# Performance work log

Measured on AMD Instinct MI355X. Metric: run time of the kernel, lower is better.

Reference implementation:

```python
import jax, jax.numpy as jnp
import numpy as np

N_HEAD = 12
M_HIST = 5      # Anderson history window (AndersonAcceleration.m)
BETA = 1.0      # Anderson mixing (AndersonAcceleration.beta)
LN_EPS = 1e-5


def _layer_norm(x, w, b):
    mu = x.mean(-1, keepdims=True)
    xc = x - mu
    var = (xc * xc).mean(-1, keepdims=True)
    return xc * jax.lax.rsqrt(var + LN_EPS) * w + b


def _mha(x, wqkv, bqkv, wo, bo):
    # torch nn.MultiheadAttention, batch_first, self-attention, no mask, dropout=0
    B, T, C = x.shape
    dh = C // N_HEAD
    qkv = x @ wqkv.T + bqkv                       # [B,T,3C]
    q, k, v = jnp.split(qkv, 3, axis=-1)
    def heads(t):
        return t.reshape(B, T, N_HEAD, dh).transpose(0, 2, 1, 3)  # [B,H,T,dh]
    q, k, v = heads(q), heads(k), heads(v)
    scores = jnp.einsum('bhqd,bhkd->bhqk', q, k) / jnp.sqrt(jnp.asarray(dh, x.dtype))
    att = jax.nn.softmax(scores, axis=-1)
    out = jnp.einsum('bhqk,bhkd->bhqd', att, v).transpose(0, 2, 1, 3).reshape(B, T, C)
    return out @ wo.T + bo


def _deq_delta(z, u, emb_row, ln1_w, ln1_b, in_proj_w, in_proj_b, out_proj_w,
               out_proj_b, ln2_w, ln2_b, mlp_w1, mlp_b1, mlp_w2, mlp_b2):
    # DEQOperator.forward -> delta_z
    z_temporal = z + 0.1 * emb_row                 # broadcast [C] over [B,T,C]
    z_ctx = z_temporal + u
    x = _layer_norm(z_ctx, ln1_w, ln1_b)
    attn_out = _mha(x, in_proj_w, in_proj_b, out_proj_w, out_proj_b)
    z_attn = z + attn_out
    h = _layer_norm(z_attn, ln2_w, ln2_b)
    h = jax.nn.gelu(h @ mlp_w1.T + mlp_b1, approximate=False) @ mlp_w2.T + mlp_b2
    z_mlp = z_attn + h
    return z_mlp - z


def _deq_solve(u, iter_emb, ln1_w, ln1_b, in_proj_w, in_proj_b, out_proj_w,
               out_proj_b, ln2_w, ln2_b, mlp_w1, mlp_b1, mlp_w2, mlp_b2, num_iters):
    B, T, C = u.shape
    z = jnp.zeros_like(u)
    Xs, Fs = [], []   # Anderson history of states / residuals
    max_row = iter_emb.shape[0] - 1
    for it in range(num_iters):
        emb_row = iter_emb[min(it, max_row)]
        delta = _deq_delta(z, u, emb_row, ln1_w, ln1_b, in_proj_w, in_proj_b,
                           out_proj_w, out_proj_b, ln2_w, ln2_b,
                           mlp_w1, mlp_b1, mlp_w2, mlp_b2)
        res = delta  # residual of f(z) = z + delta_z w.r.t. z
        Xs.append(z); Fs.append(res)
        if len(Xs) > M_HIST:
            Xs.pop(0); Fs.pop(0)
        if len(Xs) == 1:
            z = z + BETA * res
        else:
            K = len(Xs) - 1
            dF = jnp.stack(Fs[:-1], 0) - res[None]               # [K,B,T,C]
            dF_f = dF.transpose(1, 2, 0, 3).reshape(B * T, K, C)  # per-token LS
            r_f = res.reshape(B * T, C)
            G = jnp.einsum('nkc,nlc->nkl', dF_f, dF_f)            # [BT,K,K]
            G = G + 1e-6 * jnp.eye(K, dtype=u.dtype)
            bvec = jnp.einsum('nkc,nc->nk', dF_f, r_f)            # [BT,K]
            alpha = jnp.linalg.solve(G, bvec[..., None])[..., 0]
            d = r_f - jnp.einsum('nkc,nk->nc', dF_f, alpha)
            z = (z.reshape(B * T, C) + BETA * d).reshape(B, T, C)
    return z


def setup_inputs() -> dict:
    key = jax.random.key(0)
    ks = jax.random.split(key, 6)
    B, T, C = 4, 1024, 768
    std = 0.02
    return {
        'u': jax.random.normal(ks[0], (B, T, C), jnp.float32),
        'iter_emb': std * jax.random.normal(ks[1], (31, C), jnp.float32),
        'ln1_w': jnp.ones((C,), jnp.float32),
        'ln1_b': jnp.zeros((C,), jnp.float32),
        'in_proj_w': std * jax.random.normal(ks[2], (3 * C, C), jnp.float32),
        'in_proj_b': jnp.zeros((3 * C,), jnp.float32),
        'out_proj_w': std * jax.random.normal(ks[3], (C, C), jnp.float32),
        'out_proj_b': jnp.zeros((C,), jnp.float32),
        'ln2_w': jnp.ones((C,), jnp.float32),
        'ln2_b': jnp.zeros((C,), jnp.float32),
        'mlp_w1': std * jax.random.normal(ks[4], (4 * C, C), jnp.float32),
        'mlp_b1': jnp.zeros((4 * C,), jnp.float32),
        'mlp_w2': std * jax.random.normal(ks[5], (C, 4 * C), jnp.float32),
        'mlp_b2': jnp.zeros((C,), jnp.float32),
        'num_iters': 6,
    }


def reference(u, iter_emb, ln1_w, ln1_b, in_proj_w, in_proj_b, out_proj_w,
              out_proj_b, ln2_w, ln2_b, mlp_w1, mlp_b1, mlp_w2, mlp_b2, num_iters):
    return _deq_solve(u, iter_emb, ln1_w, ln1_b, in_proj_w, in_proj_b,
                      out_proj_w, out_proj_b, ln2_w, ln2_b,
                      mlp_w1, mlp_b1, mlp_w2, mlp_b2, int(num_iters))
```

## Files before the change

kernel.cpp:

```cpp
#include <hip/hip_runtime.h>
#include <math.h>

#define BT 4096
#define CDIM 768
#define NHEAD 12
#define DH 64
#define TSEQ 1024
#define BBATCH 4

typedef _Float16 f16;
typedef __attribute__((ext_vector_type(4))) _Float16 f16x4;
typedef __attribute__((ext_vector_type(8))) _Float16 f16x8;
typedef __attribute__((ext_vector_type(4))) float f32x4;

__device__ __forceinline__ void gload_lds16(const f16* g, f16* l) {
  __builtin_amdgcn_global_load_lds(
      (const __attribute__((address_space(1))) unsigned*)(const void*)g,
      (__attribute__((address_space(3))) unsigned*)(void*)l, 16, 0, 0);
}

__device__ __forceinline__ float block_reduce_sum(float v, float* sbuf) {
#pragma unroll
  for (int o = 32; o > 0; o >>= 1) v += __shfl_down(v, o, 64);
  int lane = threadIdx.x & 63;
  int w = threadIdx.x >> 6;
  if (lane == 0) sbuf[w] = v;
  __syncthreads();
  float r = sbuf[0] + sbuf[1] + sbuf[2] + sbuf[3];
  __syncthreads();
  return r;
}

__global__ __launch_bounds__(256) void zero_kernel(float4* __restrict__ p) {
  p[(size_t)blockIdx.x * 256 + threadIdx.x] = make_float4(0.f, 0.f, 0.f, 0.f);
}

__global__ __launch_bounds__(256) void cvt_f16_kernel(
    const float* __restrict__ in, f16* __restrict__ out) {
  size_t i = ((size_t)blockIdx.x * 256 + threadIdx.x) * 4;
  float4 v = *(const float4*)(in + i);
  f16x4 o = {(f16)v.x, (f16)v.y, (f16)v.z, (f16)v.w};
  *(f16x4*)(out + i) = o;
}

__global__ __launch_bounds__(256) void ln1_kernel(
    const float* __restrict__ z, const float* __restrict__ u,
    const float* __restrict__ emb, const float* __restrict__ w,
    const float* __restrict__ b, f16* __restrict__ x) {
  __shared__ float sbuf[4];
  int row = blockIdx.x;
  int tid = threadIdx.x;
  const float* zr = z + (size_t)row * CDIM;
  const float* ur = u + (size_t)row * CDIM;
  float v[3];
  float s = 0.f;
#pragma unroll
  for (int i = 0; i < 3; i++) {
    int c = tid + i * 256;
    v[i] = zr[c] + 0.1f * emb[c] + ur[c];
    s += v[i];
  }
  s = block_reduce_sum(s, sbuf);
  float mu = s * (1.f / CDIM);
  float sq = 0.f;
#pragma unroll
  for (int i = 0; i < 3; i++) { v[i] -= mu; sq += v[i] * v[i]; }
  sq = block_reduce_sum(sq, sbuf);
  float rstd = rsqrtf(sq * (1.f / CDIM) + 1e-5f);
  f16* xr = x + (size_t)row * CDIM;
#pragma unroll
  for (int i = 0; i < 3; i++) {
    int c = tid + i * 256;
    xr[c] = (f16)(v[i] * rstd * w[c] + b[c]);
  }
}

__global__ __launch_bounds__(256) void ln2_kernel(
    const float* __restrict__ in, const float* __restrict__ w,
    const float* __restrict__ b, f16* __restrict__ x) {
  __shared__ float sbuf[4];
  int row = blockIdx.x;
  int tid = threadIdx.x;
  const float* ir = in + (size_t)row * CDIM;
  float v[3];
  float s = 0.f;
#pragma unroll
  for (int i = 0; i < 3; i++) {
    int c = tid + i * 256;
    v[i] = ir[c];
    s += v[i];
  }
  s = block_reduce_sum(s, sbuf);
  float mu = s * (1.f / CDIM);
  float sq = 0.f;
#pragma unroll
  for (int i = 0; i < 3; i++) { v[i] -= mu; sq += v[i] * v[i]; }
  sq = block_reduce_sum(sq, sbuf);
  float rstd = rsqrtf(sq * (1.f / CDIM) + 1e-5f);
  f16* xr = x + (size_t)row * CDIM;
#pragma unroll
  for (int i = 0; i < 3; i++) {
    int c = tid + i * 256;
    xr[c] = (f16)(v[i] * rstd * w[c] + b[c]);
  }
}

__device__ __forceinline__ float gelu_exact(float t) {
  return 0.5f * t * (1.f + erff(t * 0.70710678118654752f));
}

template <int MODE>
__global__ __launch_bounds__(256, 3) void gemm_mfma(
    const f16* __restrict__ A, const f16* __restrict__ W,
    const float* __restrict__ bias, f16* __restrict__ hq,
    f16* __restrict__ hk, f16* __restrict__ hvt, f16* __restrict__ hout,
    int M, int N, int K) {
  __shared__ __align__(16) f16 As[128 * 32];
  __shared__ __align__(16) f16 Bs[128 * 32];
  int tid = threadIdx.x;
  int wv = tid >> 6, lane = tid & 63;
  int bm = blockIdx.y, bn = blockIdx.x;
  int wm = (wv >> 1) * 64, wn = (wv & 1) * 64;

  int srow = wv * 16 + (lane >> 2);
  int scol = (lane & 3) * 8;
  const f16* gA = A + (size_t)(bm * 128 + srow) * K + scol;
  const f16* gB = W + (size_t)(bn * 128 + srow) * K + scol;
  f16* lA = As + wv * 16 * 32;
  f16* lB = Bs + wv * 16 * 32;

  f32x4 acc[4][4];
#pragma unroll
  for (int i = 0; i < 4; i++)
#pragma unroll
    for (int j = 0; j < 4; j++) acc[i][j] = (f32x4){0.f, 0.f, 0.f, 0.f};

  int arow = lane & 15;
  int koff = (lane >> 4) * 8;

  for (int k0 = 0; k0 < K; k0 += 32) {
    __syncthreads();
    gload_lds16(gA + k0, lA);
    gload_lds16(gA + (size_t)64 * K + k0, lA + 64 * 32);
    gload_lds16(gB + k0, lB);
    gload_lds16(gB + (size_t)64 * K + k0, lB + 64 * 32);
    __syncthreads();
    f16x8 af[4], bfr[4];
#pragma unroll
    for (int mi = 0; mi < 4; mi++)
      af[mi] = *(const f16x8*)&As[(wm + mi * 16 + arow) * 32 + koff];
#pragma unroll
    for (int nj = 0; nj < 4; nj++)
      bfr[nj] = *(const f16x8*)&Bs[(wn + nj * 16 + arow) * 32 + koff];
#pragma unroll
    for (int mi = 0; mi < 4; mi++)
#pragma unroll
      for (int nj = 0; nj < 4; nj++)
        acc[mi][nj] = __builtin_amdgcn_mfma_f32_16x16x32_f16(
            af[mi], bfr[nj], acc[mi][nj], 0, 0, 0);
  }

  int crow0 = bm * 128 + wm + (lane >> 4) * 4;
  int ccol0 = bn * 128 + wn + (lane & 15);
#pragma unroll
  for (int nj = 0; nj < 4; nj++) {
    int col = ccol0 + nj * 16;
    float bcol = bias[col];
    if constexpr (MODE == 3) {
      int which = col / CDIM;
      int rem = col - which * CDIM;
      int h = rem >> 6;
      int d = rem & 63;
#pragma unroll
      for (int mi = 0; mi < 4; mi++) {
#pragma unroll
        for (int r = 0; r < 4; r++) {
          int m = crow0 + mi * 16 + r;
          int bb = m >> 10, t = m & 1023;
          f16 val = (f16)(acc[mi][nj][r] + bcol);
          if (which == 0)
            hq[(((size_t)(bb * NHEAD + h) * TSEQ + t) << 6) + d] = val;
          else if (which == 1)
            hk[(((size_t)(bb * NHEAD + h) * TSEQ + t) << 6) + d] = val;
          else
            hvt[(((size_t)(bb * NHEAD + h) * DH + d) << 10) + t] = val;
        }
      }
    } else {
#pragma unroll
      for (int mi = 0; mi < 4; mi++) {
#pragma unroll
        for (int r = 0; r < 4; r++) {
          int m = crow0 + mi * 16 + r;
          size_t idx = (size_t)m * N + col;
          hout[idx] = (f16)gelu_exact(acc[mi][nj][r] + bcol);
        }
      }
    }
  }
}

#define GS 72
template <int MODE>
__global__ __launch_bounds__(256, 4) void gemm_mfma64(
    const f16* __restrict__ A, const f16* __restrict__ W,
    const float* __restrict__ bias, const float* __restrict__ aux1,
    const float* __restrict__ aux2, float* __restrict__ fout0,
    int M, int N, int K) {
  __shared__ __align__(16) f16 As[64 * GS];
  __shared__ __align__(16) f16 Bs[64 * GS];
  int tid = threadIdx.x;
  int wv = tid >> 6, lane = tid & 63;
  int bm = blockIdx.x, bn = blockIdx.y;
  int wm = (wv >> 1) * 32, wn = (wv & 1) * 32;

  int srow = tid >> 2;
  int scol = (tid & 3) * 16;
  const f16* gA = A + (size_t)(bm * 64 + srow) * K + scol;
  const f16* gB = W + (size_t)(bn * 64 + srow) * K + scol;

  f32x4 acc[2][2];
#pragma unroll
  for (int i = 0; i < 2; i++)
#pragma unroll
    for (int j = 0; j < 2; j++) acc[i][j] = (f32x4){0.f, 0.f, 0.f, 0.f};

  int am = lane & 15;
  int ak = (lane >> 4) * 8;

  f16x8 a0 = *(const f16x8*)(gA);
  f16x8 a1 = *(const f16x8*)(gA + 8);
  f16x8 b0 = *(const f16x8*)(gB);
  f16x8 b1 = *(const f16x8*)(gB + 8);

  for (int k0 = 0; k0 < K; k0 += 64) {
    __syncthreads();
    *(f16x8*)&As[srow * GS + scol] = a0;
    *(f16x8*)&As[srow * GS + scol + 8] = a1;
    *(f16x8*)&Bs[srow * GS + scol] = b0;
    *(f16x8*)&Bs[srow * GS + scol + 8] = b1;
    __syncthreads();
    int kn = k0 + 64;
    if (kn < K) {
      a0 = *(const f16x8*)(gA + kn);
      a1 = *(const f16x8*)(gA + kn + 8);
      b0 = *(const f16x8*)(gB + kn);
      b1 = *(const f16x8*)(gB + kn + 8);
    }
#pragma unroll
    for (int kk = 0; kk < 2; kk++) {
      f16x8 af[2], bfr[2];
#pragma unroll
      for (int mi = 0; mi < 2; mi++)
        af[mi] = *(const f16x8*)&As[(wm + mi * 16 + am) * GS + kk * 32 + ak];
#pragma unroll
      for (int nj = 0; nj < 2; nj++)
        bfr[nj] = *(const f16x8*)&Bs[(wn + nj * 16 + am) * GS + kk * 32 + ak];
#pragma unroll
      for (int mi = 0; mi < 2; mi++)
#pragma unroll
        for (int nj = 0; nj < 2; nj++)
          acc[mi][nj] = __builtin_amdgcn_mfma_f32_16x16x32_f16(
              af[mi], bfr[nj], acc[mi][nj], 0, 0, 0);
    }
  }

  int crow0 = bm * 64 + wm + (lane >> 4) * 4;
  int ccol0 = bn * 64 + wn + (lane & 15);
#pragma unroll
  for (int nj = 0; nj < 2; nj++) {
    int col = ccol0 + nj * 16;
    float bcol = bias[col];
#pragma unroll
    for (int mi = 0; mi < 2; mi++) {
#pragma unroll
      for (int r = 0; r < 4; r++) {
        int m = crow0 + mi * 16 + r;
        size_t idx = (size_t)m * N + col;
        float val = acc[mi][nj][r] + bcol;
        if constexpr (MODE == 0) {
          fout0[idx] = val + aux1[idx];
        } else {
          fout0[idx] = val + aux1[idx] - aux2[idx];
        }
      }
    }
  }
}

#define PSTRIDE 72
#define KVS 72
__global__ __launch_bounds__(256, 3) void flash_attn8(
    const f16* __restrict__ Qg, const f16* __restrict__ Kg,
    const f16* __restrict__ Vt, f16* __restrict__ attn) {
  __shared__ __align__(16) f16 Ks[64 * KVS];
  __shared__ __align__(16) f16 Vs[64 * KVS];
  __shared__ __align__(16) f16 Plds[4][16 * PSTRIDE];
  int tid = threadIdx.x;
  int wv = tid >> 6, lane = tid & 63;
  int bh = blockIdx.x;
  int bb = bh / NHEAD, h = bh % NHEAD;
  int m0 = (blockIdx.y * 4 + wv) * 16;
  int am = lane & 15;
  int quad = lane >> 4;
  int ak = quad * 8;

  int srow = tid >> 3;
  int scol = (tid & 7) * 8;

  const f16* kb = Kg + (((size_t)bh * TSEQ) << 6);
  const f16* vb = Vt + (((size_t)bh * DH) << 10);

  const f16* qbase = Qg + (((size_t)bh * TSEQ + m0) << 6);
  f16x8 qf0 = *(const f16x8*)(qbase + am * 64 + ak);
  f16x8 qf1 = *(const f16x8*)(qbase + am * 64 + 32 + ak);
#pragma unroll
  for (int i = 0; i < 8; i++) { qf0[i] *= (f16)0.125f; qf1[i] *= (f16)0.125f; }

  f16* Pw = Plds[wv];
  f32x4 Oa[4];
#pragma unroll
  for (int i = 0; i < 4; i++) Oa[i] = (f32x4){0.f, 0.f, 0.f, 0.f};
  float lpart[4] = {0.f, 0.f, 0.f, 0.f};

  f16x8 kr0 = *(const f16x8*)(kb + (size_t)srow * 64 + scol);
  f16x8 kr1 = *(const f16x8*)(kb + (size_t)(32 + srow) * 64 + scol);
  f16x8 vr0 = *(const f16x8*)(vb + (size_t)srow * TSEQ + scol);
  f16x8 vr1 = *(const f16x8*)(vb + (size_t)(32 + srow) * TSEQ + scol);

  for (int n0 = 0; n0 < TSEQ; n0 += 64) {
    __syncthreads();
    *(f16x8*)&Ks[srow * KVS + scol] = kr0;
    *(f16x8*)&Ks[(32 + srow) * KVS + scol] = kr1;
    *(f16x8*)&Vs[srow * KVS + scol] = vr0;
    *(f16x8*)&Vs[(32 + srow) * KVS + scol] = vr1;
    __syncthreads();
    int nn = n0 + 64;
    if (nn < TSEQ) {
      kr0 = *(const f16x8*)(kb + (size_t)(nn + srow) * 64 + scol);
      kr1 = *(const f16x8*)(kb + (size_t)(nn + 32 + srow) * 64 + scol);
      vr0 = *(const f16x8*)(vb + (size_t)srow * TSEQ + nn + scol);
      vr1 = *(const f16x8*)(vb + (size_t)(32 + srow) * TSEQ + nn + scol);
    }
    f32x4 S[4];
#pragma unroll
    for (int t = 0; t < 4; t++) {
      f16x8 kf0 = *(const f16x8*)&Ks[(16 * t + am) * KVS + ak];
      f16x8 kf1 = *(const f16x8*)&Ks[(16 * t + am) * KVS + 32 + ak];
      S[t] = __builtin_amdgcn_mfma_f32_16x16x32_f16(
          qf0, kf0, (f32x4){0.f, 0.f, 0.f, 0.f}, 0, 0, 0);
      S[t] = __builtin_amdgcn_mfma_f32_16x16x32_f16(qf1, kf1, S[t], 0, 0, 0);
    }
#pragma unroll
    for (int t = 0; t < 4; t++) {
#pragma unroll
      for (int r = 0; r < 4; r++) {
        float p = __expf(S[t][r]);
        lpart[r] += p;
        Pw[(quad * 4 + r) * PSTRIDE + 16 * t + am] = (f16)p;
      }
    }
    f16x8 pa0 = *(const f16x8*)&Pw[am * PSTRIDE + ak];
    f16x8 pa1 = *(const f16x8*)&Pw[am * PSTRIDE + 32 + ak];
#pragma unroll
    for (int dt = 0; dt < 4; dt++) {
      f16x8 vf0 = *(const f16x8*)&Vs[(16 * dt + am) * KVS + ak];
      f16x8 vf1 = *(const f16x8*)&Vs[(16 * dt + am) * KVS + 32 + ak];
      Oa[dt] = __builtin_amdgcn_mfma_f32_16x16x32_f16(pa0, vf0, Oa[dt], 0, 0, 0);
      Oa[dt] = __builtin_amdgcn_mfma_f32_16x16x32_f16(pa1, vf1, Oa[dt], 0, 0, 0);
    }
  }

#pragma unroll
  for (int o = 1; o < 16; o <<= 1)
#pragma unroll
    for (int r = 0; r < 4; r++) lpart[r] += __shfl_xor(lpart[r], o, 64);

#pragma unroll
  for (int r = 0; r < 4; r++) {
    int m = m0 + quad * 4 + r;
    float inv = 1.f / lpart[r];
    f16* orow = attn + ((size_t)(bb * TSEQ + m)) * CDIM + h * DH;
#pragma unroll
    for (int dt = 0; dt < 4; dt++)
      orow[dt * 16 + am] = (f16)(Oa[dt][r] * inv);
  }
}

__global__ __launch_bounds__(256) void add_res_kernel(
    float* __restrict__ z, const float* __restrict__ r) {
  size_t i = (size_t)blockIdx.x * 256 + threadIdx.x;
  z[i] += r[i];
}

template <int KA>
__global__ __launch_bounds__(256) void anderson_kernel(
    float* __restrict__ z, const float* __restrict__ rescur,
    const float* __restrict__ p0, const float* __restrict__ p1,
    const float* __restrict__ p2, const float* __restrict__ p3) {
  __shared__ float sbuf[4];
  int row = blockIdx.x, tid = threadIdx.x;
  size_t base = (size_t)row * CDIM + tid;
  float r[3];
#pragma unroll
  for (int i = 0; i < 3; i++) r[i] = rescur[base + i * 256];
  const float* ps[4] = {p0, p1, p2, p3};
  float dF[KA][3];
#pragma unroll
  for (int k = 0; k < KA; k++)
#pragma unroll
    for (int i = 0; i < 3; i++) dF[k][i] = ps[k][base + i * 256] - r[i];

  float Gm[KA][KA], bv[KA];
#pragma unroll
  for (int k = 0; k < KA; k++) {
#pragma unroll
    for (int ll = k; ll < KA; ll++) {
      float p = 0.f;
#pragma unroll
      for (int i = 0; i < 3; i++) p += dF[k][i] * dF[ll][i];
      float t = block_reduce_sum(p, sbuf);
      Gm[k][ll] = t;
      Gm[ll][k] = t;
    }
  }
#pragma unroll
  for (int k = 0; k < KA; k++) Gm[k][k] += 1e-6f;
#pragma unroll
  for (int k = 0; k < KA; k++) {
    float p = 0.f;
#pragma unroll
    for (int i = 0; i < 3; i++) p += dF[k][i] * r[i];
    bv[k] = block_reduce_sum(p, sbuf);
  }
  float alpha[KA];
#pragma unroll
  for (int p = 0; p < KA; p++) {
    float inv = 1.f / Gm[p][p];
#pragma unroll
    for (int rr = p + 1; rr < KA; rr++) {
      float f = Gm[rr][p] * inv;
#pragma unroll
      for (int c = p; c < KA; c++) Gm[rr][c] -= f * Gm[p][c];
      bv[rr] -= f * bv[p];
    }
  }
#pragma unroll
  for (int p = KA - 1; p >= 0; p--) {
    float s2 = bv[p];
#pragma unroll
    for (int c = p + 1; c < KA; c++) s2 -= Gm[p][c] * alpha[c];
    alpha[p] = s2 / Gm[p][p];
  }
#pragma unroll
  for (int i = 0; i < 3; i++) {
    float d = r[i];
#pragma unroll
    for (int k = 0; k < KA; k++) d = fmaf(-dF[k][i], alpha[k], d);
    z[base + i * 256] += d;
  }
}

extern "C" void kernel_launch(void* const* d_in, const int* in_sizes, int n_in,
                              void* d_out, int out_size, void* d_ws,
                              size_t ws_size, hipStream_t stream) {
  (void)in_sizes; (void)n_in; (void)out_size; (void)ws_size;
  const float* u = (const float*)d_in[0];
  const float* iter_emb = (const float*)d_in[1];
  const float* ln1w = (const float*)d_in[2];
  const float* ln1b = (const float*)d_in[3];
  const float* wqkv = (const float*)d_in[4];
  const float* bqkv = (const float*)d_in[5];
  const float* wo = (const float*)d_in[6];
  const float* bo = (const float*)d_in[7];
  const float* ln2w = (const float*)d_in[8];
  const float* ln2b = (const float*)d_in[9];
  const float* w1 = (const float*)d_in[10];
  const float* b1 = (const float*)d_in[11];
  const float* w2 = (const float*)d_in[12];
  const float* b2 = (const float*)d_in[13];

  const size_t S = (size_t)BT * CDIM;
  float* ws = (float*)d_ws;
  float* z = ws + 0 * S;
  float* zattn = ws + 1 * S;
  float* res[5] = {ws + 2 * S, ws + 3 * S, ws + 4 * S, ws + 5 * S, ws + 6 * S};
  f16* q_h = (f16*)(ws + 7 * S);
  f16* k_h = q_h + S;
  f16* vt_h = q_h + 2 * S;
  f16* h_h = (f16*)(ws + 7 * S);
  f16* x_h = (f16*)(ws + 9 * S);
  f16* wqkv_h = x_h + S;
  f16* wo_h = wqkv_h + (size_t)3 * CDIM * CDIM;
  f16* w1_h = wo_h + (size_t)CDIM * CDIM;
  f16* w2_h = w1_h + (size_t)4 * CDIM * CDIM;

  cvt_f16_kernel<<<1728, 256, 0, stream>>>(wqkv, wqkv_h);
  cvt_f16_kernel<<<576, 256, 0, stream>>>(wo, wo_h);
  cvt_f16_kernel<<<2304, 256, 0, stream>>>(w1, w1_h);
  cvt_f16_kernel<<<2304, 256, 0, stream>>>(w2, w2_h);
  zero_kernel<<<S / 1024, 256, 0, stream>>>((float4*)z);

  for (int it = 0; it < 6; it++) {
    ln1_kernel<<<BT, 256, 0, stream>>>(z, u, iter_emb + it * CDIM, ln1w, ln1b,
                                       x_h);
    gemm_mfma<3><<<dim3(18, 32), 256, 0, stream>>>(
        x_h, wqkv_h, bqkv, q_h, k_h, vt_h, nullptr, BT, 3 * CDIM, CDIM);
    flash_attn8<<<dim3(BBATCH * NHEAD, TSEQ / 64), 256, 0, stream>>>(
        q_h, k_h, vt_h, x_h);
    gemm_mfma64<0><<<dim3(64, 12), 256, 0, stream>>>(
        x_h, wo_h, bo, z, nullptr, zattn, BT, CDIM, CDIM);
    ln2_kernel<<<BT, 256, 0, stream>>>(zattn, ln2w, ln2b, x_h);
    gemm_mfma<1><<<dim3(24, 32), 256, 0, stream>>>(
        x_h, w1_h, b1, nullptr, nullptr, nullptr, h_h, BT, 4 * CDIM, CDIM);
    float* rcur = res[it % 5];
    gemm_mfma64<2><<<dim3(64, 12), 256, 0, stream>>>(
        h_h, w2_h, b2, zattn, z, rcur, BT, CDIM, 4 * CDIM);

    int Kh = it < 4 ? it : 4;
    if (Kh == 0) {
      add_res_kernel<<<S / 256, 256, 0, stream>>>(z, rcur);
    } else {
      const float* p[4] = {rcur, rcur, rcur, rcur};
      for (int kx = 1; kx <= Kh; kx++) p[kx - 1] = res[(it - kx) % 5];
      switch (Kh) {
        case 1: anderson_kernel<1><<<BT, 256, 0, stream>>>(z, rcur, p[0], p[1], p[2], p[3]); break;
        case 2: anderson_kernel<2><<<BT, 256, 0, stream>>>(z, rcur, p[0], p[1], p[2], p[3]); break;
        case 3: anderson_kernel<3><<<BT, 256, 0, stream>>>(z, rcur, p[0], p[1], p[2], p[3]); break;
        default: anderson_kernel<4><<<BT, 256, 0, stream>>>(z, rcur, p[0], p[1], p[2], p[3]); break;
      }
    }
  }
  hipMemcpyAsync(d_out, z, S * sizeof(float), hipMemcpyDeviceToDevice, stream);
}
```

Before: 1.243 ms.

## Prefetch GEMM tiles through registers with padded LDS and BK=64

Replaces the direct global-to-LDS loads in the MFMA GEMM with register-staged loads. The next K-tile is prefetched into registers while the current tile is consumed from LDS. The K step is doubled to 64 and LDS rows are padded to 72 halves to avoid bank conflicts on the fragment reads. The aim is to hide global load latency and halve barrier count, at the cost of more registers and more LDS, which may lower occupancy under the 3-blocks-per-CU bound.

```diff
diff --git a/kernel.cpp b/kernel.cpp
--- a/kernel.cpp
+++ b/kernel.cpp
@@ -12,12 +12,6 @@
 typedef __attribute__((ext_vector_type(4))) _Float16 f16x4;
 typedef __attribute__((ext_vector_type(8))) _Float16 f16x8;
 typedef __attribute__((ext_vector_type(4))) float f32x4;
-
-__device__ __forceinline__ void gload_lds16(const f16* g, f16* l) {
-  __builtin_amdgcn_global_load_lds(
-      (const __attribute__((address_space(1))) unsigned*)(const void*)g,
-      (__attribute__((address_space(3))) unsigned*)(void*)l, 16, 0, 0);
-}
 
 __device__ __forceinline__ float block_reduce_sum(float v, float* sbuf) {
 #pragma unroll
@@ -109,25 +103,24 @@
   return 0.5f * t * (1.f + erff(t * 0.70710678118654752f));
 }
 
+#define GS128 72
 template <int MODE>
 __global__ __launch_bounds__(256, 3) void gemm_mfma(
     const f16* __restrict__ A, const f16* __restrict__ W,
     const float* __restrict__ bias, f16* __restrict__ hq,
     f16* __restrict__ hk, f16* __restrict__ hvt, f16* __restrict__ hout,
     int M, int N, int K) {
-  __shared__ __align__(16) f16 As[128 * 32];
-  __shared__ __align__(16) f16 Bs[128 * 32];
+  __shared__ __align__(16) f16 As[128 * GS128];
+  __shared__ __align__(16) f16 Bs[128 * GS128];
   int tid = threadIdx.x;
   int wv = tid >> 6, lane = tid & 63;
   int bm = blockIdx.y, bn = blockIdx.x;
   int wm = (wv >> 1) * 64, wn = (wv & 1) * 64;
 
-  int srow = wv * 16 + (lane >> 2);
-  int scol = (lane & 3) * 8;
+  int srow = tid >> 3;
+  int scol = (tid & 7) * 8;
   const f16* gA = A + (size_t)(bm * 128 + srow) * K + scol;
   const f16* gB = W + (size_t)(bn * 128 + srow) * K + scol;
-  f16* lA = As + wv * 16 * 32;
-  f16* lB = Bs + wv * 16 * 32;
 
   f32x4 acc[4][4];
 #pragma unroll
@@ -135,33 +128,53 @@
 #pragma unroll
     for (int j = 0; j < 4; j++) acc[i][j] = (f32x4){0.f, 0.f, 0.f, 0.f};
 
-  int arow = lane & 15;
-  int koff = (lane >> 4) * 8;
-
-  for (int k0 = 0; k0 < K; k0 += 32) {
+  int am = lane & 15;
+  int quad = lane >> 4;
+  int ak = quad * 8;
+
+  f16x8 ar[4], br[4];
+#pragma unroll
+  for (int c = 0; c < 4; c++) {
+    ar[c] = *(const f16x8*)(gA + (size_t)(c * 32) * K);
+    br[c] = *(const f16x8*)(gB + (size_t)(c * 32) * K);
+  }
+
+  for (int k0 = 0; k0 < K; k0 += 64) {
     __syncthreads();
-    gload_lds16(gA + k0, lA);
-    gload_lds16(gA + (size_t)64 * K + k0, lA + 64 * 32);
-    gload_lds16(gB + k0, lB);
-    gload_lds16(gB + (size_t)64 * K + k0, lB + 64 * 32);
+#pragma unroll
+    for (int c = 0; c < 4; c++) {
+      *(f16x8*)&As[(srow + c * 32) * GS128 + scol] = ar[c];
+      *(f16x8*)&Bs[(srow + c * 32) * GS128 + scol] = br[c];
+    }
     __syncthreads();
-    f16x8 af[4], bfr[4];
-#pragma unroll
-    for (int mi = 0; mi < 4; mi++)
-      af[mi] = *(const f16x8*)&As[(wm + mi * 16 + arow) * 32 + koff];
-#pragma unroll
-    for (int nj = 0; nj < 4; nj++)
-      bfr[nj] = *(const f16x8*)&Bs[(wn + nj * 16 + arow) * 32 + koff];
-#pragma unroll
-    for (int mi = 0; mi < 4; mi++)
+    int kn = k0 + 64;
+    if (kn < K) {
+#pragma unroll
+      for (int c = 0; c < 4; c++) {
+        ar[c] = *(const f16x8*)(gA + (size_t)(c * 32) * K + kn);
+        br[c] = *(const f16x8*)(gB + (size_t)(c * 32) * K + kn);
+      }
+    }
+#pragma unroll
+    for (int kk = 0; kk < 2; kk++) {
+      f16x8 af[4], bfr[4];
+#pragma unroll
+      for (int mi = 0; mi < 4; mi++)
+        af[mi] = *(const f16x8*)&As[(wm + mi * 16 + am) * GS128 + kk * 32 + ak];
 #pragma unroll
       for (int nj = 0; nj < 4; nj++)
-        acc[mi][nj] = __builtin_amdgcn_mfma_f32_16x16x32_f16(
-            af[mi], bfr[nj], acc[mi][nj], 0, 0, 0);
-  }
-
-  int crow0 = bm * 128 + wm + (lane >> 4) * 4;
-  int ccol0 = bn * 128 + wn + (lane & 15);
+        bfr[nj] = *(const f16x8*)&Bs[(wn + nj * 16 + am) * GS128 + kk * 32 + ak];
+#pragma unroll
+      for (int mi = 0; mi < 4; mi++)
+#pragma unroll
+        for (int nj = 0; nj < 4; nj++)
+          acc[mi][nj] = __builtin_amdgcn_mfma_f32_16x16x32_f16(
+              af[mi], bfr[nj], acc[mi][nj], 0, 0, 0);
+    }
+  }
+
+  int crow0 = bm * 128 + wm + quad * 4;
+  int ccol0 = bn * 128 + wn + am;
 #pragma unroll
   for (int nj = 0; nj < 4; nj++) {
     int col = ccol0 + nj * 16;
```

Measured after the change: 1.238 ms. No clear change (-0.5%).
